# Performance work log

Measured on AMD Instinct MI355X. Metric: run time of the kernel, lower is better.

Reference implementation:

```python
import jax, jax.numpy as jnp
import numpy as np

B, L, D, N = 2, 8192, 1024, 512
EPS = 1e-5


def setup_inputs() -> dict:
    key = jax.random.key(0)
    ks = jax.random.split(key, 6)
    x = jax.random.normal(ks[0], (B, L, D), dtype=jnp.float32)
    Lambda_real = jax.random.normal(ks[1], (N,), dtype=jnp.float32)
    Lambda_imag = jax.random.normal(ks[2], (N,), dtype=jnp.float32)
    C_real = jax.random.normal(ks[3], (D, N), dtype=jnp.float32)
    C_imag = jax.random.normal(ks[4], (D, N), dtype=jnp.float32)
    param_D = jax.random.normal(ks[5], (D,), dtype=jnp.float32)
    gamma = jnp.ones((D,), dtype=jnp.float32)   # LayerNorm weight
    beta = jnp.zeros((D,), dtype=jnp.float32)   # LayerNorm bias
    return {"x": x, "Lambda_real": Lambda_real, "Lambda_imag": Lambda_imag,
            "C_real": C_real, "C_imag": C_imag, "param_D": param_D,
            "gamma": gamma, "beta": beta}


def reference(x, Lambda_real, Lambda_imag, C_real, C_imag, param_D, gamma, beta):
    seq_len = x.shape[1]
    # LayerNorm over last dim (biased variance, eps=1e-5, elementwise affine)
    mean = jnp.mean(x, axis=-1, keepdims=True)
    var = jnp.mean(jnp.square(x - mean), axis=-1, keepdims=True)
    u = (x - mean) * jax.lax.rsqrt(var + EPS) * gamma + beta   # [b, l, d]
    residual = u * param_D                                      # [b, l, d]
    # Diagonal SSM kernel synthesis
    Lam = -jnp.exp(Lambda_real) + 1j * jnp.exp(Lambda_imag)     # [n] complex
    C = (C_real + 1j * C_imag) * (jnp.exp(Lam) - 1.0) / Lam     # [d, n]
    ar = jnp.arange(seq_len, dtype=jnp.float32)
    S = jnp.exp(Lam[:, None] * ar[None, :])                     # [n, l] Vandermonde-like
    K = jnp.einsum('hn,nl->lh', C, S).real                      # [l, d]
    # FFT long convolution (linear conv via 2L zero-padding)
    n_fft = seq_len * 2
    u_f = jnp.fft.rfft(u, n=n_fft, axis=-2)                     # [b, l+1, d]
    K_f = jnp.fft.rfft(K, n=n_fft, axis=-2)                     # [l+1, d]
    y = jnp.fft.irfft(u_f * K_f, n=n_fft, axis=-2)[..., :seq_len, :]
    return y + residual
```

## Files before the change

### kernel.cpp

```cpp
#include <hip/hip_runtime.h>
#include <math.h>

#define LLEN 8192
#define DDIM 1024
#define NB   2
#define NMODE 512
#define MFFT 8192
#define SLEN 4096
#define KF_STRIDE 8208

#define PIDX(i) ((i) + ((i) >> 4))
#define FBUF 8704

#define OFF_UT   ((size_t)0)
#define OFF_KF   ((size_t)67108864)
#define OFF_KT   ((size_t)134348800)
#define OFF_CPK  ((size_t)167903232)
#define OFF_MEAN ((size_t)172097536)
#define OFF_RSTD ((size_t)172163072)
#define OFF_LAMR ((size_t)172228608)
#define OFF_LAMID ((size_t)172230656)
#define OFF_WR   ((size_t)172234752)
#define OFF_WI   ((size_t)172236800)
#define OFF_CUT  ((size_t)172238848)
#define OFF_TW   ((size_t)172240896)
#define OFF_TWR  ((size_t)172306432)
#define OFF_SORTN ((size_t)172371976)
#define OFF_TCNT  ((size_t)172374024)
#define WS_NEED  ((size_t)172374088)

#define OFF_SP   OFF_KF

__global__ __launch_bounds__(256) void ln_stats_kernel(const float* __restrict__ x,
                                                       float* __restrict__ mean,
                                                       float* __restrict__ rstd) {
  __shared__ float red[16];
  int row = blockIdx.x;
  int tid = threadIdx.x;
  const float4* xr = (const float4*)(x + (size_t)row * DDIM);
  float4 v = xr[tid];
  float s = v.x + v.y + v.z + v.w;
  float q = v.x*v.x + v.y*v.y + v.z*v.z + v.w*v.w;
  #pragma unroll
  for (int off = 32; off; off >>= 1) { s += __shfl_down(s, off); q += __shfl_down(q, off); }
  int wid = tid >> 6;
  if ((tid & 63) == 0) { red[wid] = s; red[8 + wid] = q; }
  __syncthreads();
  if (tid == 0) {
    float ts = red[0] + red[1] + red[2] + red[3];
    float tq = red[8] + red[9] + red[10] + red[11];
    float m = ts * (1.0f / DDIM);
    float var = tq * (1.0f / DDIM) - m * m;
    mean[row] = m;
    rstd[row] = rsqrtf(var + 1e-5f);
  }
}

__global__ __launch_bounds__(256) void transpose_ln_kernel(const float* __restrict__ x,
                                                           const float* __restrict__ mean,
                                                           const float* __restrict__ rstd,
                                                           const float* __restrict__ gamma,
                                                           const float* __restrict__ beta,
                                                           float* __restrict__ uT) {
  __shared__ float tile[32][33];
  int lt = blockIdx.x * 32, dt = blockIdx.y * 32, b = blockIdx.z;
  int c = threadIdx.x & 31, r0 = threadIdx.x >> 5;
  float gv = gamma[dt + c], bv = beta[dt + c];
  #pragma unroll
  for (int i = 0; i < 4; i++) {
    int r = r0 + i * 8;
    float m = mean[(size_t)b * LLEN + lt + r];
    float rs = rstd[(size_t)b * LLEN + lt + r];
    float xv = x[((size_t)b * LLEN + lt + r) * DDIM + dt + c];
    tile[r][c] = (xv - m) * rs * gv + bv;
  }
  __syncthreads();
  #pragma unroll
  for (int i = 0; i < 4; i++) {
    int r = r0 + i * 8;
    uT[((size_t)b * DDIM + dt + r) * LLEN + lt + c] = tile[c][r];
  }
}

__global__ void build_tables_kernel(const float* __restrict__ Lr, const float* __restrict__ Li,
                                    float* lamr, double* lamid, float* wre, float* wim, int* cut,
                                    float2* twH, float2* twR) {
  int gid = blockIdx.x * 256 + threadIdx.x;
  if (gid < NMODE) {
    double lr = (double)Lr[gid], li = (double)Li[gid];
    double ar = -exp(lr);
    double ai = exp(li);
    lamr[gid] = (float)ar;
    lamid[gid] = ai;
    double em = exp(ar);
    double cs = cos(ai), sn = sin(ai);
    double er = em * cs - 1.0;
    double ei = em * sn;
    double den = ar * ar + ai * ai;
    wre[gid] = (float)((er * ar + ei * ai) / den);
    wim[gid] = (float)((ei * ar - er * ai) / den);
    int co = (int)(40.0 / (-ar)) + 1;
    cut[gid] = co > SLEN ? SLEN : co;
  }
  int j = gid - NMODE;
  if (j >= 0 && j < 8192) {
    if (j == 0) {
      twH[0] = make_float2(1.f, 0.f);
    } else {
      int lev = 31 - __clz(j);
      int Ls = 1 << lev;
      int p = j - Ls;
      double a = 3.14159265358979323846264338 * (double)p / (double)Ls;
      twH[j] = make_float2((float)cos(a), (float)sin(a));
    }
  }
  int k = gid - (NMODE + 8192);
  if (k >= 0 && k <= 8192) {
    double a = 6.283185307179586476925287 * (double)k / 16384.0;
    twR[k] = make_float2((float)cos(a), (float)sin(a));
  }
}

#define KB4_LT 256
#define NTILE (SLEN / KB4_LT)
__global__ __launch_bounds__(NMODE) void sortmodes_kernel(const int* __restrict__ cut,
                                                          int* __restrict__ sortn,
                                                          int* __restrict__ tcount) {
  __shared__ int sc[NMODE];
  int tid = threadIdx.x;
  sc[tid] = cut[tid];
  __syncthreads();
  int c = sc[tid];
  int rank = 0;
  for (int m = 0; m < NMODE; ++m) {
    int cm = sc[m];
    rank += (cm > c) || (cm == c && m < tid);
  }
  sortn[rank] = tid;
  if (tid < NTILE) {
    int l0 = tid * KB4_LT;
    int cnt = 0;
    for (int m = 0; m < NMODE; ++m) cnt += (sc[m] > l0);
    tcount[tid] = cnt;
  }
}

__global__ __launch_bounds__(256) void cpack_kernel(const float* __restrict__ Cr,
                                                    const float* __restrict__ Ci,
                                                    const float* __restrict__ wre,
                                                    const float* __restrict__ wim,
                                                    const int* __restrict__ sortn,
                                                    float2* __restrict__ Cpk) {
  int idx = blockIdx.x * 256 + threadIdx.x;
  int r = idx >> 10, d = idx & (DDIM - 1);
  int n = sortn[r];
  float cr = Cr[(size_t)d * NMODE + n], ci = Ci[(size_t)d * NMODE + n];
  float wr = wre[n], wi = wim[n];
  Cpk[idx] = make_float2(cr * wr - ci * wi, cr * wi + ci * wr);
}

__global__ __launch_bounds__(256) void sbuild_kernel(const float* __restrict__ lamr,
                                                     const double* __restrict__ lamid,
                                                     const int* __restrict__ cut,
                                                     const int* __restrict__ sortn,
                                                     float2* __restrict__ Spack) {
  int r = blockIdx.y;
  int n = sortn[r];
  int l = blockIdx.x * 256 + threadIdx.x;
  float sr = 0.f, si = 0.f;
  if (l < cut[n]) {
    float mag = expf(lamr[n] * (float)l);
    double ph = lamid[n] * (double)l;
    const double tp = 6.283185307179586476925287;
    const double itp = 1.0 / 6.283185307179586476925287;
    ph -= floor(ph * itp) * tp;
    float cs, sn; sincosf((float)ph, &sn, &cs);
    sr = mag * cs; si = mag * sn;
  }
  Spack[(size_t)r * SLEN + l] = make_float2(sr, si);
}

#define KB5_DT 4
__global__ __launch_bounds__(256) void kbuild7_kernel(const float2* __restrict__ Spack,
                                                      const float2* __restrict__ Cpk,
                                                      const int* __restrict__ tcount,
                                                      float* __restrict__ KT) {
  __shared__ float2 sC[NMODE][KB5_DT];
  int t = blockIdx.y;
  int d0 = blockIdx.x * KB5_DT;
  int tid = threadIdx.x;
  int nact = tcount[t];
  for (int i = tid; i < nact * KB5_DT; i += 256) {
    int r = i >> 2, dd = i & 3;
    sC[r][dd] = Cpk[(size_t)r * DDIM + d0 + dd];
  }
  __syncthreads();
  int l = t * KB4_LT + tid;
  float acc0 = 0.f, acc1 = 0.f, acc2 = 0.f, acc3 = 0.f;
  const float2* sp = Spack + l;
  int i = 0;
  int n8 = nact & ~7;
  for (; i < n8; i += 8) {
    const float2* p = sp + (size_t)i * SLEN;
    float2 s0 = p[0];
    float2 s1 = p[(size_t)1 * SLEN];
    float2 s2 = p[(size_t)2 * SLEN];
    float2 s3 = p[(size_t)3 * SLEN];
    float2 s4 = p[(size_t)4 * SLEN];
    float2 s5 = p[(size_t)5 * SLEN];
    float2 s6 = p[(size_t)6 * SLEN];
    float2 s7 = p[(size_t)7 * SLEN];
    #define KACC(ss, rr) { \
      float2 c0 = sC[rr][0], c1 = sC[rr][1], c2 = sC[rr][2], c3 = sC[rr][3]; \
      acc0 += ss.x * c0.x - ss.y * c0.y; \
      acc1 += ss.x * c1.x - ss.y * c1.y; \
      acc2 += ss.x * c2.x - ss.y * c2.y; \
      acc3 += ss.x * c3.x - ss.y * c3.y; }
    KACC(s0, i + 0) KACC(s1, i + 1) KACC(s2, i + 2) KACC(s3, i + 3)
    KACC(s4, i + 4) KACC(s5, i + 5) KACC(s6, i + 6) KACC(s7, i + 7)
  }
  for (; i < nact; ++i) {
    float2 s0 = sp[(size_t)i * SLEN];
    KACC(s0, i)
  }
  #undef KACC
  KT[(size_t)(d0 + 0) * SLEN + l] = acc0;
  KT[(size_t)(d0 + 1) * SLEN + l] = acc1;
  KT[(size_t)(d0 + 2) * SLEN + l] = acc2;
  KT[(size_t)(d0 + 3) * SLEN + l] = acc3;
}

__device__ __forceinline__ void fft8192_core(float2* buf0, float2* buf1,
                                             const float2* __restrict__ twH,
                                             int tid, float sign) {
  float2* src = buf0;
  float2* dst = buf1;
  #pragma unroll 1
  for (int s = 0; s < 12; s += 2) {
    int L = 1 << s;
    __syncthreads();
    #pragma unroll
    for (int it = 0; it < 2; ++it) {
      int j = tid + it * 1024;
      int p = j & (L - 1);
      int q = j >> s;
      float2 w1 = twH[L + p];
      float2 w2 = twH[2 * L + p];
      float w1r = w1.x, w1i = sign * w1.y;
      float w2r = w2.x, w2i = sign * w2.y;
      float2 x0 = src[PIDX(j)];
      float2 x1 = src[PIDX(j + 4096)];
      float2 x2 = src[PIDX(j + 2048)];
      float2 x3 = src[PIDX(j + 6144)];
      float t1r = w1r * x1.x - w1i * x1.y, t1i = w1r * x1.y + w1i * x1.x;
      float t3r = w1r * x3.x - w1i * x3.y, t3i = w1r * x3.y + w1i * x3.x;
      float Ar = x0.x + t1r, Ai = x0.y + t1i;
      float Cr = x0.x - t1r, Ci = x0.y - t1i;
      float Br = x2.x + t3r, Bi = x2.y + t3i;
      float Dr = x2.x - t3r, Di = x2.y - t3i;
      float Er = w2r * Br - w2i * Bi, Ei = w2r * Bi + w2i * Br;
      float Fr = w2r * Dr - w2i * Di, Fi = w2r * Di + w2i * Dr;
      int o = (q << (s + 2)) + p;
      dst[PIDX(o)]         = make_float2(Ar + Er, Ai + Ei);
      dst[PIDX(o + L)]     = make_float2(Cr - sign * Fi, Ci + sign * Fr);
      dst[PIDX(o + 2*L)]   = make_float2(Ar - Er, Ai - Ei);
      dst[PIDX(o + 3*L)]   = make_float2(Cr + sign * Fi, Ci - sign * Fr);
    }
    float2* t = src; src = dst; dst = t;
  }
  __syncthreads();
  #pragma unroll
  for (int it = 0; it < 4; ++it) {
    int j = tid + it * 1024;
    float2 w = twH[4096 + j];
    float wr = w.x, wi = sign * w.y;
    float2 a = src[PIDX(j)];
    float2 b = src[PIDX(j + 4096)];
    float br = wr * b.x - wi * b.y;
    float bi = wr * b.y + wi * b.x;
    dst[PIDX(j)]        = make_float2(a.x + br, a.y + bi);
    dst[PIDX(j + 4096)] = make_float2(a.x - br, a.y - bi);
  }
  __syncthreads();
}

__global__ __launch_bounds__(1024) void kf_fft_kernel(const float* __restrict__ KT,
                                                      const float2* __restrict__ twH,
                                                      const float2* __restrict__ twR,
                                                      float2* __restrict__ Kf) {
  __shared__ float2 bufA[FBUF];
  __shared__ float2 bufB[FBUF];
  int d = blockIdx.x;
  int tid = threadIdx.x;
  const float2* row = (const float2*)(KT + (size_t)d * SLEN);
  for (int j = tid; j < MFFT; j += 1024)
    bufA[PIDX(j)] = (j < SLEN / 2) ? row[j] : make_float2(0.f, 0.f);
  fft8192_core(bufA, bufB, twH, tid, -1.f);
  const float scale = 1.0f / 8192.0f;
  float2* out = Kf + (size_t)d * KF_STRIDE;
  for (int k = tid; k <= 4096; k += 1024) {
    if (k == 0) {
      float2 z0 = bufB[PIDX(0)];
      out[0]    = make_float2((z0.x + z0.y) * scale, 0.f);
      out[8192] = make_float2((z0.x - z0.y) * scale, 0.f);
    } else {
      float2 zk = bufB[PIDX(k)];
      float2 zm = bufB[PIDX(MFFT - k)];
      float Ar = 0.5f * (zk.x + zm.x), Ai = 0.5f * (zk.y - zm.y);
      float Br = 0.5f * (zk.x - zm.x), Bi = 0.5f * (zk.y + zm.y);
      float2 t = twR[k];
      float c = t.x, sn = t.y;
      float e1r = sn * Br - c * Bi;
      float e1i = sn * Bi + c * Br;
      out[k]        = make_float2((Ar - e1r) * scale, (Ai - e1i) * scale);
      out[MFFT - k] = make_float2((Ar + e1r) * scale, (-Ai - e1i) * scale);
    }
  }
}

__global__ __launch_bounds__(1024) void conv_fft_kernel(float* __restrict__ uT,
                                                        const float2* __restrict__ twH,
                                                        const float2* __restrict__ twR,
                                                        const float2* __restrict__ Kf,
                                                        const float* __restrict__ pD) {
  __shared__ float2 bufA[FBUF];
  __shared__ float2 bufB[FBUF];
  int wg = blockIdx.x;
  int b = wg >> 10, d = wg & (DDIM - 1);
  int tid = threadIdx.x;
  float2* row = (float2*)(uT + ((size_t)b * DDIM + d) * LLEN);
  for (int j = tid; j < MFFT; j += 1024)
    bufA[PIDX(j)] = (j < 4096) ? row[j] : make_float2(0.f, 0.f);
  fft8192_core(bufA, bufB, twH, tid, -1.f);
  const float2* kf = Kf + (size_t)d * KF_STRIDE;
  for (int k = tid; k <= 4096; k += 1024) {
    if (k == 0) {
      float2 z0 = bufB[PIDX(0)];
      float U0 = z0.x + z0.y;
      float UM = z0.x - z0.y;
      float Y0 = U0 * kf[0].x;
      float YM = UM * kf[8192].x;
      bufA[PIDX(0)] = make_float2(0.5f * (Y0 + YM), 0.5f * (Y0 - YM));
    } else {
      float2 zk = bufB[PIDX(k)];
      float2 zm = bufB[PIDX(MFFT - k)];
      float Ar = 0.5f * (zk.x + zm.x), Ai = 0.5f * (zk.y - zm.y);
      float Br = 0.5f * (zk.x - zm.x), Bi = 0.5f * (zk.y + zm.y);
      float2 t = twR[k];
      float c = t.x, sn = t.y;
      float e1r = sn * Br - c * Bi;
      float e1i = sn * Bi + c * Br;
      float Ukr = Ar - e1r, Uki = Ai - e1i;
      float Umr = Ar + e1r, Umi = -Ai - e1i;
      float2 kk = kf[k], km = kf[MFFT - k];
      float Ykr = Ukr * kk.x - Uki * kk.y, Yki = Ukr * kk.y + Uki * kk.x;
      float Ymr = Umr * km.x - Umi * km.y, Ymi = Umr * km.y + Umi * km.x;
      float Eyr = 0.5f * (Ykr + Ymr), Eyi = 0.5f * (Yki - Ymi);
      float Byr = 0.5f * (Ykr - Ymr), Byi = 0.5f * (Yki + Ymi);
      bufA[PIDX(k)]        = make_float2(Eyr - sn * Byr - c * Byi, Eyi + c * Byr - sn * Byi);
      bufA[PIDX(MFFT - k)] = make_float2(Eyr + sn * Byr + c * Byi, -Eyi + c * Byr - sn * Byi);
    }
  }
  __syncthreads();
  fft8192_core(bufA, bufB, twH, tid, +1.f);
  float pdv = pD[d];
  for (int j = tid; j < 4096; j += 1024) {
    float2 uv = row[j];
    float2 yv = bufB[PIDX(j)];
    row[j] = make_float2(yv.x + uv.x * pdv, yv.y + uv.y * pdv);
  }
}

__global__ __launch_bounds__(256) void final_kernel(const float* __restrict__ yT,
                                                    float* __restrict__ out) {
  __shared__ float tile[32][33];
  int lt = blockIdx.x * 32, dt = blockIdx.y * 32, b = blockIdx.z;
  int c = threadIdx.x & 31, r0 = threadIdx.x >> 5;
  #pragma unroll
  for (int i = 0; i < 4; i++) {
    int r = r0 + i * 8;
    tile[r][c] = yT[((size_t)b * DDIM + dt + r) * LLEN + lt + c];
  }
  __syncthreads();
  #pragma unroll
  for (int i = 0; i < 4; i++) {
    int r = r0 + i * 8;
    out[((size_t)b * LLEN + lt + r) * DDIM + dt + c] = tile[c][r];
  }
}

extern "C" void kernel_launch(void* const* d_in, const int* in_sizes, int n_in,
                              void* d_out, int out_size, void* d_ws, size_t ws_size,
                              hipStream_t stream) {
  (void)in_sizes; (void)n_in; (void)out_size;
  if (ws_size < WS_NEED) return;
  const float* x     = (const float*)d_in[0];
  const float* Lr    = (const float*)d_in[1];
  const float* Li    = (const float*)d_in[2];
  const float* Cr    = (const float*)d_in[3];
  const float* Ci    = (const float*)d_in[4];
  const float* pD    = (const float*)d_in[5];
  const float* gamma = (const float*)d_in[6];
  const float* beta  = (const float*)d_in[7];
  float* out = (float*)d_out;
  char* ws = (char*)d_ws;

  float*  UT    = (float*)(ws + OFF_UT);
  float2* KF    = (float2*)(ws + OFF_KF);
  float2* SPK   = (float2*)(ws + OFF_SP);
  float*  KT    = (float*)(ws + OFF_KT);
  float2* CPK   = (float2*)(ws + OFF_CPK);
  float*  MEAN  = (float*)(ws + OFF_MEAN);
  float*  RSTD  = (float*)(ws + OFF_RSTD);
  float*  LAMR  = (float*)(ws + OFF_LAMR);
  double* LAMID = (double*)(ws + OFF_LAMID);
  float*  WRe   = (float*)(ws + OFF_WR);
  float*  WIm   = (float*)(ws + OFF_WI);
  int*    CUT   = (int*)(ws + OFF_CUT);
  float2* TWH   = (float2*)(ws + OFF_TW);
  float2* TWR   = (float2*)(ws + OFF_TWR);
  int*    SORTN = (int*)(ws + OFF_SORTN);
  int*    TCNT  = (int*)(ws + OFF_TCNT);

  ln_stats_kernel<<<NB * LLEN, 256, 0, stream>>>(x, MEAN, RSTD);
  transpose_ln_kernel<<<dim3(LLEN / 32, DDIM / 32, NB), 256, 0, stream>>>(x, MEAN, RSTD, gamma, beta, UT);
  build_tables_kernel<<<67, 256, 0, stream>>>(Lr, Li, LAMR, LAMID, WRe, WIm, CUT, TWH, TWR);
  sortmodes_kernel<<<1, NMODE, 0, stream>>>(CUT, SORTN, TCNT);
  cpack_kernel<<<(NMODE * DDIM) / 256, 256, 0, stream>>>(Cr, Ci, WRe, WIm, SORTN, CPK);
  sbuild_kernel<<<dim3(SLEN / 256, NMODE), 256, 0, stream>>>(LAMR, LAMID, CUT, SORTN, SPK);
  kbuild7_kernel<<<dim3(DDIM / KB5_DT, NTILE), 256, 0, stream>>>(SPK, CPK, TCNT, KT);
  kf_fft_kernel<<<DDIM, 1024, 0, stream>>>(KT, TWH, TWR, KF);
  conv_fft_kernel<<<NB * DDIM, 1024, 0, stream>>>(UT, TWH, TWR, KF, pD);
  final_kernel<<<dim3(LLEN / 32, DDIM / 32, NB), 256, 0, stream>>>(UT, out);
}
```

Measured before the change: 345.2 us.

## Switch shared-memory FFT stages from radix-4 to radix-8 passes

The 8192-point in-LDS FFT core now runs four radix-8 passes instead of six radix-4 passes before the final radix-2 stage. Each thread loads eight points, does three butterfly levels in registers, then writes back. This cuts shared-memory round trips and `__syncthreads` barriers per transform. The cost is higher register pressure per thread and a more complex twiddle indexing scheme that must stay correct.

```diff
diff --git a/kernel.cpp b/kernel.cpp
--- a/kernel.cpp
+++ b/kernel.cpp
@@ -236,35 +236,62 @@
   float2* src = buf0;
   float2* dst = buf1;
   #pragma unroll 1
-  for (int s = 0; s < 12; s += 2) {
+  for (int s = 0; s < 12; s += 3) {
     int L = 1 << s;
     __syncthreads();
-    #pragma unroll
-    for (int it = 0; it < 2; ++it) {
-      int j = tid + it * 1024;
-      int p = j & (L - 1);
-      int q = j >> s;
-      float2 w1 = twH[L + p];
-      float2 w2 = twH[2 * L + p];
-      float w1r = w1.x, w1i = sign * w1.y;
-      float w2r = w2.x, w2i = sign * w2.y;
-      float2 x0 = src[PIDX(j)];
-      float2 x1 = src[PIDX(j + 4096)];
-      float2 x2 = src[PIDX(j + 2048)];
-      float2 x3 = src[PIDX(j + 6144)];
-      float t1r = w1r * x1.x - w1i * x1.y, t1i = w1r * x1.y + w1i * x1.x;
-      float t3r = w1r * x3.x - w1i * x3.y, t3i = w1r * x3.y + w1i * x3.x;
-      float Ar = x0.x + t1r, Ai = x0.y + t1i;
-      float Cr = x0.x - t1r, Ci = x0.y - t1i;
-      float Br = x2.x + t3r, Bi = x2.y + t3i;
-      float Dr = x2.x - t3r, Di = x2.y - t3i;
-      float Er = w2r * Br - w2i * Bi, Ei = w2r * Bi + w2i * Br;
-      float Fr = w2r * Dr - w2i * Di, Fi = w2r * Di + w2i * Dr;
-      int o = (q << (s + 2)) + p;
-      dst[PIDX(o)]         = make_float2(Ar + Er, Ai + Ei);
-      dst[PIDX(o + L)]     = make_float2(Cr - sign * Fi, Ci + sign * Fr);
-      dst[PIDX(o + 2*L)]   = make_float2(Ar - Er, Ai - Ei);
-      dst[PIDX(o + 3*L)]   = make_float2(Cr + sign * Fi, Ci - sign * Fr);
+    int j = tid;
+    int p = j & (L - 1);
+    int q = j >> s;
+    float2 x0 = src[PIDX(j)];
+    float2 x1 = src[PIDX(j + 1024)];
+    float2 x2 = src[PIDX(j + 2048)];
+    float2 x3 = src[PIDX(j + 3072)];
+    float2 x4 = src[PIDX(j + 4096)];
+    float2 x5 = src[PIDX(j + 5120)];
+    float2 x6 = src[PIDX(j + 6144)];
+    float2 x7 = src[PIDX(j + 7168)];
+    float2 w1 = twH[L + p];
+    float w1r = w1.x, w1i = sign * w1.y;
+    float t4r = w1r*x4.x - w1i*x4.y, t4i = w1r*x4.y + w1i*x4.x;
+    float t5r = w1r*x5.x - w1i*x5.y, t5i = w1r*x5.y + w1i*x5.x;
+    float t6r = w1r*x6.x - w1i*x6.y, t6i = w1r*x6.y + w1i*x6.x;
+    float t7r = w1r*x7.x - w1i*x7.y, t7i = w1r*x7.y + w1i*x7.x;
+    float A0r = x0.x + t4r, A0i = x0.y + t4i, B0r = x0.x - t4r, B0i = x0.y - t4i;
+    float A1r = x1.x + t5r, A1i = x1.y + t5i, B1r = x1.x - t5r, B1i = x1.y - t5i;
+    float A2r = x2.x + t6r, A2i = x2.y + t6i, B2r = x2.x - t6r, B2i = x2.y - t6i;
+    float A3r = x3.x + t7r, A3i = x3.y + t7i, B3r = x3.x - t7r, B3i = x3.y - t7i;
+    int O = (q << (s + 3)) + p;
+    {
+      float2 wa = twH[2*L + p];  float war = wa.x, wai = sign * wa.y;
+      float2 wb = twH[4*L + p];  float wbr = wb.x, wbi = sign * wb.y;
+      float t1r_ = war*A2r - wai*A2i, t1i_ = war*A2i + wai*A2r;
+      float t3r_ = war*A3r - wai*A3i, t3i_ = war*A3i + wai*A3r;
+      float Ar = A0r + t1r_, Ai = A0i + t1i_;
+      float Cr = A0r - t1r_, Ci = A0i - t1i_;
+      float Br = A1r + t3r_, Bi = A1i + t3i_;
+      float Dr = A1r - t3r_, Di = A1i - t3i_;
+      float Er = wbr*Br - wbi*Bi, Ei = wbr*Bi + wbi*Br;
+      float Fr = wbr*Dr - wbi*Di, Fi = wbr*Di + wbi*Dr;
+      dst[PIDX(O)]         = make_float2(Ar + Er, Ai + Ei);
+      dst[PIDX(O + 2*L)]   = make_float2(Cr - sign*Fi, Ci + sign*Fr);
+      dst[PIDX(O + 4*L)]   = make_float2(Ar - Er, Ai - Ei);
+      dst[PIDX(O + 6*L)]   = make_float2(Cr + sign*Fi, Ci - sign*Fr);
+    }
+    {
+      float2 wa = twH[3*L + p];  float war = wa.x, wai = sign * wa.y;
+      float2 wb = twH[5*L + p];  float wbr = wb.x, wbi = sign * wb.y;
+      float t1r_ = war*B2r - wai*B2i, t1i_ = war*B2i + wai*B2r;
+      float t3r_ = war*B3r - wai*B3i, t3i_ = war*B3i + wai*B3r;
+      float Ar = B0r + t1r_, Ai = B0i + t1i_;
+      float Cr = B0r - t1r_, Ci = B0i - t1i_;
+      float Br = B1r + t3r_, Bi = B1i + t3i_;
+      float Dr = B1r - t3r_, Di = B1i - t3i_;
+      float Er = wbr*Br - wbi*Bi, Ei = wbr*Bi + wbi*Br;
+      float Fr = wbr*Dr - wbi*Di, Fi = wbr*Di + wbi*Dr;
+      dst[PIDX(O + L)]     = make_float2(Ar + Er, Ai + Ei);
+      dst[PIDX(O + 3*L)]   = make_float2(Cr - sign*Fi, Ci + sign*Fr);
+      dst[PIDX(O + 5*L)]   = make_float2(Ar - Er, Ai - Ei);
+      dst[PIDX(O + 7*L)]   = make_float2(Cr + sign*Fi, Ci - sign*Fr);
     }
     float2* t = src; src = dst; dst = t;
   }
```

After: 312.2 us. 9.6% less time.

## Switch 8192-point FFT to radix-8 stages with fused load and final radix-2

Applied to the files above, without the earlier changes.

Replaces the radix-4 shared-memory FFT (six radix-4 passes plus one radix-2 pass) with four radix-8 passes and a final radix-2 step. The first stage reads directly from global memory and exploits the known zero padding. The last radix-2 butterfly is folded into the real-FFT post-processing or into the output write. This reduces the number of shared-memory round trips and barriers per FFT, at the cost of higher register pressure with 1024-thread blocks. It also leaves a redundant Byi computation in place.

```diff
diff --git a/kernel.cpp b/kernel.cpp
--- a/kernel.cpp
+++ b/kernel.cpp
@@ -230,58 +230,84 @@
   KT[(size_t)(d0 + 3) * SLEN + l] = acc3;
 }
 
-__device__ __forceinline__ void fft8192_core(float2* buf0, float2* buf1,
-                                             const float2* __restrict__ twH,
-                                             int tid, float sign) {
-  float2* src = buf0;
-  float2* dst = buf1;
-  #pragma unroll 1
-  for (int s = 0; s < 12; s += 2) {
-    int L = 1 << s;
-    __syncthreads();
-    #pragma unroll
-    for (int it = 0; it < 2; ++it) {
-      int j = tid + it * 1024;
-      int p = j & (L - 1);
-      int q = j >> s;
-      float2 w1 = twH[L + p];
-      float2 w2 = twH[2 * L + p];
-      float w1r = w1.x, w1i = sign * w1.y;
-      float w2r = w2.x, w2i = sign * w2.y;
-      float2 x0 = src[PIDX(j)];
-      float2 x1 = src[PIDX(j + 4096)];
-      float2 x2 = src[PIDX(j + 2048)];
-      float2 x3 = src[PIDX(j + 6144)];
-      float t1r = w1r * x1.x - w1i * x1.y, t1i = w1r * x1.y + w1i * x1.x;
-      float t3r = w1r * x3.x - w1i * x3.y, t3i = w1r * x3.y + w1i * x3.x;
-      float Ar = x0.x + t1r, Ai = x0.y + t1i;
-      float Cr = x0.x - t1r, Ci = x0.y - t1i;
-      float Br = x2.x + t3r, Bi = x2.y + t3i;
-      float Dr = x2.x - t3r, Di = x2.y - t3i;
-      float Er = w2r * Br - w2i * Bi, Ei = w2r * Bi + w2i * Br;
-      float Fr = w2r * Dr - w2i * Di, Fi = w2r * Di + w2i * Dr;
-      int o = (q << (s + 2)) + p;
-      dst[PIDX(o)]         = make_float2(Ar + Er, Ai + Ei);
-      dst[PIDX(o + L)]     = make_float2(Cr - sign * Fi, Ci + sign * Fr);
-      dst[PIDX(o + 2*L)]   = make_float2(Ar - Er, Ai - Ei);
-      dst[PIDX(o + 3*L)]   = make_float2(Cr + sign * Fi, Ci - sign * Fr);
-    }
-    float2* t = src; src = dst; dst = t;
-  }
-  __syncthreads();
-  #pragma unroll
-  for (int it = 0; it < 4; ++it) {
-    int j = tid + it * 1024;
-    float2 w = twH[4096 + j];
-    float wr = w.x, wi = sign * w.y;
-    float2 a = src[PIDX(j)];
-    float2 b = src[PIDX(j + 4096)];
-    float br = wr * b.x - wi * b.y;
-    float bi = wr * b.y + wi * b.x;
-    dst[PIDX(j)]        = make_float2(a.x + br, a.y + bi);
-    dst[PIDX(j + 4096)] = make_float2(a.x - br, a.y - bi);
-  }
-  __syncthreads();
+#define R4BLK(b0, b2, b1, b3, wa, wb, o0, o1, o2, o3) { \
+  float war=(wa).x, wai=sign*(wa).y, wbr=(wb).x, wbi=sign*(wb).y; \
+  float t1r_=war*(b2).x - wai*(b2).y, t1i_=war*(b2).y + wai*(b2).x; \
+  float t3r_=war*(b3).x - wai*(b3).y, t3i_=war*(b3).y + wai*(b3).x; \
+  float Ar=(b0).x+t1r_, Ai=(b0).y+t1i_, Cr=(b0).x-t1r_, Ci=(b0).y-t1i_; \
+  float Br=(b1).x+t3r_, Bi=(b1).y+t3i_, Dr=(b1).x-t3r_, Di=(b1).y-t3i_; \
+  float Er=wbr*Br-wbi*Bi, Ei=wbr*Bi+wbi*Br; \
+  float Fr=wbr*Dr-wbi*Di, Fi=wbr*Di+wbi*Dr; \
+  dst[PIDX(o0)]=make_float2(Ar+Er,Ai+Ei); \
+  dst[PIDX(o1)]=make_float2(Cr-sign*Fi,Ci+sign*Fr); \
+  dst[PIDX(o2)]=make_float2(Ar-Er,Ai-Ei); \
+  dst[PIDX(o3)]=make_float2(Cr+sign*Fi,Ci-sign*Fr); }
+
+__device__ __forceinline__ void r8_stage(const float2* src, float2* dst,
+                                         const float2* __restrict__ twH,
+                                         int tid, float sign, int s) {
+  int L = 1 << s;
+  int j = tid;
+  int p = j & (L - 1);
+  int q = j >> s;
+  float2 x0 = src[PIDX(j)];
+  float2 x1 = src[PIDX(j + 1024)];
+  float2 x2 = src[PIDX(j + 2048)];
+  float2 x3 = src[PIDX(j + 3072)];
+  float2 x4 = src[PIDX(j + 4096)];
+  float2 x5 = src[PIDX(j + 5120)];
+  float2 x6 = src[PIDX(j + 6144)];
+  float2 x7 = src[PIDX(j + 7168)];
+  float2 w1 = twH[L + p];
+  float w1r = w1.x, w1i = sign * w1.y;
+  float t4r = w1r*x4.x - w1i*x4.y, t4i = w1r*x4.y + w1i*x4.x;
+  float t5r = w1r*x5.x - w1i*x5.y, t5i = w1r*x5.y + w1i*x5.x;
+  float t6r = w1r*x6.x - w1i*x6.y, t6i = w1r*x6.y + w1i*x6.x;
+  float t7r = w1r*x7.x - w1i*x7.y, t7i = w1r*x7.y + w1i*x7.x;
+  float2 A0 = make_float2(x0.x + t4r, x0.y + t4i), B0 = make_float2(x0.x - t4r, x0.y - t4i);
+  float2 A1 = make_float2(x1.x + t5r, x1.y + t5i), B1 = make_float2(x1.x - t5r, x1.y - t5i);
+  float2 A2 = make_float2(x2.x + t6r, x2.y + t6i), B2 = make_float2(x2.x - t6r, x2.y - t6i);
+  float2 A3 = make_float2(x3.x + t7r, x3.y + t7i), B3 = make_float2(x3.x - t7r, x3.y - t7i);
+  int O = (q << (s + 3)) + p;
+  R4BLK(A0, A2, A1, A3, twH[2*L + p], twH[4*L + p], O, O + 2*L, O + 4*L, O + 6*L)
+  R4BLK(B0, B2, B1, B3, twH[3*L + p], twH[5*L + p], O + L, O + 3*L, O + 5*L, O + 7*L)
+}
+
+__device__ __forceinline__ void r8_first4(const float2* __restrict__ g, float2* dst,
+                                          const float2* __restrict__ twH,
+                                          int tid, float sign) {
+  float2 x0 = g[tid];
+  float2 x1 = g[tid + 1024];
+  float2 x2 = g[tid + 2048];
+  float2 x3 = g[tid + 3072];
+  int O = tid << 3;
+  R4BLK(x0, x2, x1, x3, twH[2], twH[4], O, O + 2, O + 4, O + 6)
+  R4BLK(x0, x2, x1, x3, twH[3], twH[5], O + 1, O + 3, O + 5, O + 7)
+}
+
+__device__ __forceinline__ void r8_first2(const float2* __restrict__ g, float2* dst,
+                                          const float2* __restrict__ twH,
+                                          int tid, float sign) {
+  float2 x0 = g[tid];
+  float2 x1 = g[tid + 1024];
+  float2 zf = make_float2(0.f, 0.f);
+  int O = tid << 3;
+  R4BLK(x0, zf, x1, zf, twH[2], twH[4], O, O + 2, O + 4, O + 6)
+  R4BLK(x0, zf, x1, zf, twH[3], twH[5], O + 1, O + 3, O + 5, O + 7)
+}
+
+__device__ __forceinline__ void fwd_final_pair(const float2* sbuf, const float2* __restrict__ twH,
+                                               int k, float2* zk, float2* zm) {
+  float2 a1 = sbuf[PIDX(k)], b1 = sbuf[PIDX(k + 4096)];
+  float2 w1 = twH[4096 + k];
+  float br1 = w1.x*b1.x + w1.y*b1.y;
+  float bi1 = w1.x*b1.y - w1.y*b1.x;
+  *zk = make_float2(a1.x + br1, a1.y + bi1);
+  float2 a2 = sbuf[PIDX(4096 - k)], b2 = sbuf[PIDX(8192 - k)];
+  float2 w2 = twH[8192 - k];
+  float br2 = w2.x*b2.x + w2.y*b2.y;
+  float bi2 = w2.x*b2.y - w2.y*b2.x;
+  *zm = make_float2(a2.x - br2, a2.y - bi2);
 }
 
 __global__ __launch_bounds__(1024) void kf_fft_kernel(const float* __restrict__ KT,
@@ -293,19 +319,32 @@
   int d = blockIdx.x;
   int tid = threadIdx.x;
   const float2* row = (const float2*)(KT + (size_t)d * SLEN);
-  for (int j = tid; j < MFFT; j += 1024)
-    bufA[PIDX(j)] = (j < SLEN / 2) ? row[j] : make_float2(0.f, 0.f);
-  fft8192_core(bufA, bufB, twH, tid, -1.f);
+  const float sign = -1.f;
+  { float2* dst = bufA; r8_first2(row, dst, twH, tid, sign); }
+  __syncthreads();
+  r8_stage(bufA, bufB, twH, tid, sign, 3);
+  __syncthreads();
+  r8_stage(bufB, bufA, twH, tid, sign, 6);
+  __syncthreads();
+  r8_stage(bufA, bufB, twH, tid, sign, 9);
+  __syncthreads();
   const float scale = 1.0f / 8192.0f;
   float2* out = Kf + (size_t)d * KF_STRIDE;
   for (int k = tid; k <= 4096; k += 1024) {
     if (k == 0) {
-      float2 z0 = bufB[PIDX(0)];
+      float2 s0 = bufB[PIDX(0)], s4 = bufB[PIDX(4096)];
+      float2 z0 = make_float2(s0.x + s4.x, s0.y + s4.y);
       out[0]    = make_float2((z0.x + z0.y) * scale, 0.f);
       out[8192] = make_float2((z0.x - z0.y) * scale, 0.f);
     } else {
-      float2 zk = bufB[PIDX(k)];
-      float2 zm = bufB[PIDX(MFFT - k)];
+      float2 zk, zm;
+      if (k == 4096) {
+        float2 s0 = bufB[PIDX(0)], s4 = bufB[PIDX(4096)];
+        zk = make_float2(s0.x - s4.x, s0.y - s4.y);
+        zm = zk;
+      } else {
+        fwd_final_pair(bufB, twH, k, &zk, &zm);
+      }
       float Ar = 0.5f * (zk.x + zm.x), Ai = 0.5f * (zk.y - zm.y);
       float Br = 0.5f * (zk.x - zm.x), Bi = 0.5f * (zk.y + zm.y);
       float2 t = twR[k];
@@ -329,21 +368,34 @@
   int b = wg >> 10, d = wg & (DDIM - 1);
   int tid = threadIdx.x;
   float2* row = (float2*)(uT + ((size_t)b * DDIM + d) * LLEN);
-  for (int j = tid; j < MFFT; j += 1024)
-    bufA[PIDX(j)] = (j < 4096) ? row[j] : make_float2(0.f, 0.f);
-  fft8192_core(bufA, bufB, twH, tid, -1.f);
+  float sign = -1.f;
+  { float2* dst = bufA; r8_first4(row, dst, twH, tid, sign); }
+  __syncthreads();
+  r8_stage(bufA, bufB, twH, tid, sign, 3);
+  __syncthreads();
+  r8_stage(bufB, bufA, twH, tid, sign, 6);
+  __syncthreads();
+  r8_stage(bufA, bufB, twH, tid, sign, 9);
+  __syncthreads();
   const float2* kf = Kf + (size_t)d * KF_STRIDE;
   for (int k = tid; k <= 4096; k += 1024) {
     if (k == 0) {
-      float2 z0 = bufB[PIDX(0)];
+      float2 s0 = bufB[PIDX(0)], s4 = bufB[PIDX(4096)];
+      float2 z0 = make_float2(s0.x + s4.x, s0.y + s4.y);
       float U0 = z0.x + z0.y;
       float UM = z0.x - z0.y;
       float Y0 = U0 * kf[0].x;
       float YM = UM * kf[8192].x;
       bufA[PIDX(0)] = make_float2(0.5f * (Y0 + YM), 0.5f * (Y0 - YM));
     } else {
-      float2 zk = bufB[PIDX(k)];
-      float2 zm = bufB[PIDX(MFFT - k)];
+      float2 zk, zm;
+      if (k == 4096) {
+        float2 s0 = bufB[PIDX(0)], s4 = bufB[PIDX(4096)];
+        zk = make_float2(s0.x - s4.x, s0.y - s4.y);
+        zm = zk;
+      } else {
+        fwd_final_pair(bufB, twH, k, &zk, &zm);
+      }
       float Ar = 0.5f * (zk.x + zm.x), Ai = 0.5f * (zk.y - zm.y);
       float Br = 0.5f * (zk.x - zm.x), Bi = 0.5f * (zk.y + zm.y);
       float2 t = twR[k];
@@ -356,18 +408,31 @@
       float Ykr = Ukr * kk.x - Uki * kk.y, Yki = Ukr * kk.y + Uki * kk.x;
       float Ymr = Umr * km.x - Umi * km.y, Ymi = Umr * km.y + Umi * km.x;
       float Eyr = 0.5f * (Ykr + Ymr), Eyi = 0.5f * (Yki - Ymi);
-      float Byr = 0.5f * (Ykr - Ymr), Byi = 0.5f * (Yki + Ymi);
+      float Byr = 0.5f * (Ykr - Ymr), Byi = 0.5f * (Yki + Byi*0.f + Yki*0.f + Ymi);
+      Byi = 0.5f * (Yki + Ymi);
       bufA[PIDX(k)]        = make_float2(Eyr - sn * Byr - c * Byi, Eyi + c * Byr - sn * Byi);
       bufA[PIDX(MFFT - k)] = make_float2(Eyr + sn * Byr + c * Byi, -Eyi + c * Byr - sn * Byi);
     }
   }
   __syncthreads();
-  fft8192_core(bufA, bufB, twH, tid, +1.f);
+  sign = +1.f;
+  r8_stage(bufA, bufB, twH, tid, sign, 0);
+  __syncthreads();
+  r8_stage(bufB, bufA, twH, tid, sign, 3);
+  __syncthreads();
+  r8_stage(bufA, bufB, twH, tid, sign, 6);
+  __syncthreads();
+  r8_stage(bufB, bufA, twH, tid, sign, 9);
+  __syncthreads();
   float pdv = pD[d];
   for (int j = tid; j < 4096; j += 1024) {
+    float2 a = bufA[PIDX(j)];
+    float2 bq = bufA[PIDX(j + 4096)];
+    float2 w = twH[4096 + j];
+    float br = w.x * bq.x - w.y * bq.y;
+    float bi = w.x * bq.y + w.y * bq.x;
     float2 uv = row[j];
-    float2 yv = bufB[PIDX(j)];
-    row[j] = make_float2(yv.x + uv.x * pdv, yv.y + uv.y * pdv);
+    row[j] = make_float2(a.x + br + uv.x * pdv, a.y + bi + uv.y * pdv);
   }
 }
 
```

Measured after the change: 299.4 us. 1.15x faster.
